# Kernel tuning notes

Hardware: AMD Instinct MI355X
Metric: run time of the kernel (lower is better)

## Reference

```python
import jax, jax.numpy as jnp
import numpy as np
from jax import lax

B, H, W = 4, 512, 512
C_DOWN, C_UP = 256, 64
DH = DW = 32          # bottleneck feature map (H/16)
K = 512               # fixed proposal count per image (<= proposal_n_max)
NMS_THR = 0.2
MIN_DIST = 3
PROP_HALF = 5         # proposal_size(11) // 2
POOL = 7
NCLS = 4              # n_classes(3) + background


def leaky(x):
    return jnp.where(x > 0, x, 0.1 * x)


def setup_inputs() -> dict:
    key = jax.random.key(0)
    ks = jax.random.split(key, 12)
    s = lambda fan: np.float32(1.0 / np.sqrt(fan))
    return {
        "xhat": jax.random.uniform(ks[0], (B, 1, H, W), jnp.float32),
        "feat_down": jax.random.normal(ks[1], (B, C_DOWN, DH, DW), jnp.float32),
        "feat_up": jax.random.normal(ks[2], (B, C_UP, H, W), jnp.float32),
        # patch head: per-pixel => only 3x3 conv center taps contribute
        "pw1": jax.random.normal(ks[3], (256, C_DOWN), jnp.float32) * s(C_DOWN),
        "pb1": jnp.zeros((256,), jnp.float32),
        "pw2": jax.random.normal(ks[4], (256, 256), jnp.float32) * s(256),
        "pb2": jnp.zeros((256,), jnp.float32),
        "pw3": jax.random.normal(ks[5], (256, 256), jnp.float32) * s(256),
        "pb3": jnp.zeros((256,), jnp.float32),
        "pfc_w": jax.random.normal(ks[6], (2, 256), jnp.float32) * s(256),
        "pfc_b": jnp.zeros((2,), jnp.float32),
        # proposal head: full 3x3 convs on 7x7 pooled rois
        "qw1": jax.random.normal(ks[7], (256, C_UP, 3, 3), jnp.float32) * s(C_UP * 9),
        "qb1": jnp.zeros((256,), jnp.float32),
        "qw2": jax.random.normal(ks[8], (256, 256, 3, 3), jnp.float32) * s(256 * 9),
        "qb2": jnp.zeros((256,), jnp.float32),
        "qw3": jax.random.normal(ks[9], (256, 256, 3, 3), jnp.float32) * s(256 * 9),
        "qb3": jnp.zeros((256,), jnp.float32),
        "qfc_w": jax.random.normal(ks[10], (NCLS, 256), jnp.float32) * s(256),
        "qfc_b": jnp.zeros((NCLS,), jnp.float32),
    }


def reference(xhat, feat_down, feat_up, pw1, pb1, pw2, pb2, pw3, pb3, pfc_w, pfc_b,
              qw1, qb1, qw2, qb2, qw3, qb3, qfc_w, qfc_b):
    # ---- patch classifier applied per pixel (3x3 conv on 1x1 padded input == center tap)
    f = leaky(jnp.einsum('bchw,oc->bohw', feat_down, pw1) + pb1[None, :, None, None])
    f = leaky(jnp.einsum('bchw,oc->bohw', f, pw2) + pb2[None, :, None, None])
    f = leaky(jnp.einsum('bchw,oc->bohw', f, pw3) + pb3[None, :, None, None])
    plogits = jnp.einsum('bchw,oc->bohw', f, pfc_w) + pfc_b[None, :, None, None]
    patch_score = jax.nn.softmax(plogits, axis=1)[:, 1:2]                 # [B,1,DH,DW]
    patch_score = jax.image.resize(patch_score, (B, 1, H, W), 'bilinear')  # align_corners=False
    # gate belief map: bad pixels set to global mean of bad pixels
    bad = patch_score < 0.5
    nbad = jnp.maximum(jnp.sum(bad), 1).astype(xhat.dtype)
    mean_bad = jnp.sum(jnp.where(bad, xhat, 0.0)) / nbad
    bm = jnp.where(bad, mean_bad, xhat)[:, 0]                             # [B,H,W]
    # ---- belief-map NMS: local maxima above absolute threshold
    win = 2 * MIN_DIST + 1
    mp = lax.reduce_window(bm, -jnp.inf, lax.max, (1, win, win), (1, 1, 1), 'SAME')
    peak_scores = jnp.where((bm == mp) & (bm > NMS_THR), bm, -jnp.inf)
    top_s, top_i = lax.top_k(peak_scores.reshape(B, -1), K)               # [B,K]
    ys = (top_i // W).astype(jnp.int32)
    xs = (top_i % W).astype(jnp.int32)
    valid = top_s > NMS_THR
    coords = jnp.stack([xs, ys], axis=-1)                                 # (x, y)
    # ---- roi_align: 11x11 boxes around peaks, one bilinear sample per 7x7 bin center
    roi_size = 2.0 * PROP_HALF
    offs = (jnp.arange(POOL, dtype=jnp.float32) + 0.5) * (roi_size / POOL)
    px = (xs.astype(jnp.float32) - PROP_HALF)[..., None] + offs           # [B,K,7]
    py = (ys.astype(jnp.float32) - PROP_HALF)[..., None] + offs

    def sample_one(feat, py_i, px_i):
        # feat [C,H,W]; py_i/px_i [K,7] -> pooled [C,K,7,7]
        yy = jnp.broadcast_to(py_i[:, :, None], (K, POOL, POOL))
        xx = jnp.broadcast_to(px_i[:, None, :], (K, POOL, POOL))
        y0 = jnp.floor(yy); x0 = jnp.floor(xx)
        wy = yy - y0; wx = xx - x0
        y0i = jnp.clip(y0.astype(jnp.int32), 0, H - 1)
        y1i = jnp.clip(y0.astype(jnp.int32) + 1, 0, H - 1)
        x0i = jnp.clip(x0.astype(jnp.int32), 0, W - 1)
        x1i = jnp.clip(x0.astype(jnp.int32) + 1, 0, W - 1)
        g = lambda yi, xi: feat[:, yi, xi]
        return (g(y0i, x0i) * (1 - wy) * (1 - wx) + g(y0i, x1i) * (1 - wy) * wx
                + g(y1i, x0i) * wy * (1 - wx) + g(y1i, x1i) * wy * wx)

    pooled = jax.vmap(sample_one)(feat_up, py, px)                        # [B,C,K,7,7]
    pooled = pooled.transpose(0, 2, 1, 3, 4).reshape(B * K, C_UP, POOL, POOL)
    # ---- proposal classifier head
    dn = ('NCHW', 'OIHW', 'NCHW')
    h = leaky(lax.conv_general_dilated(pooled, qw1, (1, 1), 'SAME', dimension_numbers=dn) + qb1[None, :, None, None])
    h = leaky(lax.conv_general_dilated(h, qw2, (1, 1), 'SAME', dimension_numbers=dn) + qb2[None, :, None, None])
    h = leaky(lax.conv_general_dilated(h, qw3, (1, 1), 'SAME', dimension_numbers=dn) + qb3[None, :, None, None])
    h = jnp.max(h, axis=(2, 3))                                           # AdaptiveMaxPool2d(1)
    cls_logits = (h @ qfc_w.T + qfc_b).reshape(B, K, NCLS)
    return cls_logits, coords, top_s, valid
```

## Files before the change

### kernel.cpp

```cpp
#include <hip/hip_runtime.h>
#include <math.h>

typedef _Float16 half_t;
typedef half_t half8 __attribute__((ext_vector_type(8)));
typedef half_t half4 __attribute__((ext_vector_type(4)));
typedef float  f32x16 __attribute__((ext_vector_type(16)));
typedef double dbl2  __attribute__((ext_vector_type(2)));

#define BB 4
#define HH 512
#define WW 512
#define IMGPIX (HH*WW)
#define KSEL 512
#define NPROP (BB*KSEL)
#define CUP 64
#define NMS_THR 0.2f

#define OFF_S32    0
#define OFF_SUM    32768
#define OFF_CNT    32776
#define OFF_CCNT   32784
#define OFF_HIST   32800
#define ZERO_BASE  32768
#define ZERO_LEN   262176
#define OFF_PFX    294944
#define OFF_R      294976
#define OFF_BITMAP 295040
#define OFF_KEYS   426112
#define OFF_SEL    8814720
#define OFF_PROPS  8831104
#define OFF_W1     8847488
#define OFF_W2     9142400
#define OFF_W3     10322048

#define LRELU_F(x) ((x) > 0.0f ? (x) : 0.1f*(x))

__global__ __launch_bounds__(256) void repatch_k(
    const float* __restrict__ fdown,
    const float* __restrict__ pw1, const float* __restrict__ pb1,
    const float* __restrict__ pw2, const float* __restrict__ pb2,
    const float* __restrict__ pw3, const float* __restrict__ pb3,
    const float* __restrict__ pfcw, const float* __restrict__ pfcb,
    double* __restrict__ s32,
    const float* __restrict__ qw1, const float* __restrict__ qw2,
    const float* __restrict__ qw3,
    half_t* __restrict__ W1, half_t* __restrict__ W2, half_t* __restrict__ W3)
{
  if (blockIdx.x >= 512) {
    const int tot1 = 256*64*9, tot2 = 256*256*9;
    int idx = (blockIdx.x - 512)*256 + threadIdx.x;
    const float* src; half_t* dst; int IC, KS, l;
    if (idx < tot1)              { src = qw1; dst = W1; IC = 64;  KS = 4;  l = idx; }
    else if (idx < tot1 + tot2)  { src = qw2; dst = W2; IC = 256; KS = 16; l = idx - tot1; }
    else if (idx < tot1 + 2*tot2){ src = qw3; dst = W3; IC = 256; KS = 16; l = idx - tot1 - tot2; }
    else return;
    int tap = l % 9;
    int t   = l / 9;
    int ic  = t % IC;
    int oc  = t / IC;
    int ks  = ic >> 4, kin = ic & 15;
    dst[((size_t)(tap*KS + ks)*256 + oc)*16 + kin] = (half_t)src[l];
    return;
  }
  __shared__ __align__(16) double xb[8][256];
  const int t = threadIdx.x;
  const int base_px = blockIdx.x * 8;
#pragma unroll
  for (int p = 0; p < 8; ++p) {
    int px = base_px + p;
    int b = px >> 10, rem = px & 1023;
    xb[p][t] = (double)fdown[(size_t)(b*256 + t)*1024 + rem];
  }
  __syncthreads();
  const float* Ws[3] = {pw1, pw2, pw3};
  const float* Bs[3] = {pb1, pb2, pb3};
  for (int L = 0; L < 3; ++L) {
    double acc[8];
    double bias = (double)Bs[L][t];
#pragma unroll
    for (int p = 0; p < 8; ++p) acc[p] = bias;
    const float* wrow = Ws[L] + t*256;
    for (int c = 0; c < 256; c += 2) {
      double w0 = (double)wrow[c], w1 = (double)wrow[c+1];
#pragma unroll
      for (int p = 0; p < 8; ++p) {
        dbl2 xv = *(const dbl2*)&xb[p][c];
        acc[p] += w0 * xv.x;
        acc[p] += w1 * xv.y;
      }
    }
    __syncthreads();
#pragma unroll
    for (int p = 0; p < 8; ++p)
      xb[p][t] = acc[p] > 0.0 ? acc[p] : 0.1*acc[p];
    __syncthreads();
  }
  if (t < 8) {
    double l0 = (double)pfcb[0], l1 = (double)pfcb[1];
    for (int c = 0; c < 256; ++c) {
      double xv = xb[t][c];
      l0 += (double)pfcw[c]       * xv;
      l1 += (double)pfcw[256 + c] * xv;
    }
    double m  = fmax(l0, l1);
    double e0 = exp(l0 - m), e1 = exp(l1 - m);
    s32[base_px + t] = e1 / (e0 + e1);
  }
}

__device__ __forceinline__ double upsample_ps(const double* __restrict__ s32,
                                              int b, int oy, int ox)
{
  double sy = (oy + 0.5)*0.0625 - 0.5;
  double sx = (ox + 0.5)*0.0625 - 0.5;
  double fy = floor(sy), fx = floor(sx);
  double wy = sy - fy,   wx = sx - fx;
  int y0 = (int)fy, x0 = (int)fx;
  int y0i = min(max(y0,   0), 31), y1i = min(max(y0+1, 0), 31);
  int x0i = min(max(x0,   0), 31), x1i = min(max(x0+1, 0), 31);
  const double* s = s32 + b*1024;
  double v00 = s[y0i*32+x0i], v01 = s[y0i*32+x1i];
  double v10 = s[y1i*32+x0i], v11 = s[y1i*32+x1i];
  return v00*(1.0-wy)*(1.0-wx) + v01*(1.0-wy)*wx
       + v10*wy*(1.0-wx)       + v11*wy*wx;
}

__global__ __launch_bounds__(256) void mean_k(
    const float* __restrict__ xhat, const double* __restrict__ s32,
    double* __restrict__ sum, unsigned long long* __restrict__ cnt,
    unsigned long long* __restrict__ bitmap)
{
  int id = blockIdx.x*256 + threadIdx.x;
  int b = id >> 18, rem = id & (IMGPIX-1);
  int oy = rem >> 9, ox = rem & 511;
  double ps = upsample_ps(s32, b, oy, ox);
  bool bad = ps < 0.5;
  int lane = threadIdx.x & 63;
  unsigned long long bb = __ballot(bad);
  if (lane == 0) bitmap[id >> 6] = bb;
  double v = bad ? (double)xhat[id] : 0.0;
  int    c = bad ? 1 : 0;
  for (int off = 32; off; off >>= 1) {
    v += __shfl_down(v, off);
    c += __shfl_down(c, off);
  }
  __shared__ double sv[4];
  __shared__ int    sc[4];
  int w = threadIdx.x >> 6;
  if (lane == 0) { sv[w] = v; sc[w] = c; }
  __syncthreads();
  if (threadIdx.x == 0) {
    atomicAdd(sum, sv[0]+sv[1]+sv[2]+sv[3]);
    atomicAdd(cnt, (unsigned long long)(sc[0]+sc[1]+sc[2]+sc[3]));
  }
}

__global__ __launch_bounds__(512) void keyfuse_k(
    const float* __restrict__ xhat, const unsigned long long* __restrict__ bitmap,
    const double* __restrict__ sum, const unsigned long long* __restrict__ cnt,
    unsigned long long* __restrict__ keys, unsigned int* __restrict__ hist0)
{
  __shared__ float rowm[14][512];
  __shared__ float bmv[8][512];
  __shared__ float rt[512];
  __shared__ unsigned int lh[4096];
  const int tid = threadIdx.x;
  const int img = blockIdx.x >> 6;
  const int rb  = (blockIdx.x & 63) * 8;
  for (int i = tid; i < 4096; i += 512) lh[i] = 0;

  unsigned long long n = *cnt; if (n < 1) n = 1;
  const float mean = (float)(*sum / (double)n);
  const int ibase = img * IMGPIX;

  for (int r = 0; r < 14; ++r) {
    int y = rb - 3 + r;
    float v = -INFINITY;
    if (y >= 0 && y < 512) {
      int id = ibase + (y << 9) + tid;
      bool bad = (bitmap[id >> 6] >> (id & 63)) & 1ull;
      v = bad ? mean : xhat[id];
    }
    int cr = y - rb;
    if (cr >= 0 && cr < 8) bmv[cr][tid] = v;
    rt[tid] = v;
    __syncthreads();
    int lo = max(tid-3, 0), hi = min(tid+3, 511);
    float m = rt[lo];
    for (int xx = lo+1; xx <= hi; ++xx) m = fmaxf(m, rt[xx]);
    rowm[r][tid] = m;
    __syncthreads();
  }

  const int lane = tid & 63;
  for (int yy = 0; yy < 8; ++yy) {
    float mp = rowm[yy][tid];
#pragma unroll
    for (int d = 1; d < 7; ++d) mp = fmaxf(mp, rowm[yy + d][tid]);
    float v = bmv[yy][tid];
    bool cand = (v == mp) && (v > NMS_THR);
    int rem = ((rb + yy) << 9) + tid;
    unsigned int inv = (unsigned int)((IMGPIX-1) - rem);
    unsigned long long key = cand
        ? ((((unsigned long long)__float_as_uint(v)) << 18) | inv)
        : (unsigned long long)inv;
    keys[ibase + rem] = key;
    int bin = (int)(key >> 36);
    unsigned long long active = ~0ull;
    while (active) {
      int src = __ffsll((long long)active) - 1;
      int bsel = __shfl(bin, src);
      unsigned long long match = __ballot(bin == bsel) & active;
      if (lane == src) atomicAdd(&lh[bsel], (unsigned int)__popcll(match));
      active &= ~match;
    }
  }
  __syncthreads();
  for (int i = tid; i < 4096; i += 512)
    if (lh[i]) atomicAdd(&hist0[img*4096 + i], lh[i]);
}

__global__ __launch_bounds__(512) void hist_k(
    const unsigned long long* __restrict__ keys,
    const unsigned long long* __restrict__ pfx,
    unsigned int* __restrict__ hist, int shift)
{
  __shared__ unsigned int lh[4096];
  const int tid = threadIdx.x;
  for (int i = tid; i < 4096; i += 512) lh[i] = 0;
  int id = blockIdx.x*512 + tid;
  int img = blockIdx.x >> 9;
  unsigned long long key = keys[id];
  bool pred = (key >> (shift + 12)) == pfx[img];
  int bin = (int)((unsigned int)(key >> shift) & 4095u);
  __syncthreads();
  int lane = tid & 63;
  unsigned long long active = __ballot(pred);
  while (active) {
    int src = __ffsll((long long)active) - 1;
    int bsel = __shfl(bin, src);
    unsigned long long match = __ballot(bin == bsel) & active;
    if (lane == src) atomicAdd(&lh[bsel], (unsigned int)__popcll(match));
    active &= ~match;
  }
  __syncthreads();
  for (int i = tid; i < 4096; i += 512)
    if (lh[i]) atomicAdd(&hist[img*4096 + i], lh[i]);
}

__global__ __launch_bounds__(512) void scan_k(
    const unsigned int* __restrict__ hist,
    unsigned long long* __restrict__ pfx, unsigned int* __restrict__ Rbuf,
    int pass)
{
  __shared__ unsigned int lsA[512], lsB[512];
  const int b = blockIdx.x, tid = threadIdx.x;
  unsigned long long pin = (pass == 0) ? 0ull : pfx[b];
  unsigned int Rin = (pass == 0) ? (unsigned int)KSEL : Rbuf[b];
  const unsigned int* h = hist + b*4096;
  unsigned int v[8]; unsigned int loc = 0;
#pragma unroll
  for (int j = 0; j < 8; ++j) { v[j] = h[tid*8 + j]; loc += v[j]; }
  lsA[tid] = loc;
  __syncthreads();
  unsigned int* s = lsA; unsigned int* d = lsB;
  for (int dd = 1; dd < 512; dd <<= 1) {
    unsigned int val = s[tid] + ((tid + dd < 512) ? s[tid + dd] : 0u);
    d[tid] = val;
    __syncthreads();
    unsigned int* t = s; s = d; d = t;
  }
  unsigned int nxt = (tid + 1 < 512) ? s[tid + 1] : 0u;
#pragma unroll
  for (int j = 7; j >= 0; --j) {
    unsigned int sfx = nxt + v[j];
    if (sfx >= Rin && nxt < Rin) {
      pfx[b] = (pin << 12) | (unsigned long long)(unsigned int)(tid*8 + j);
      Rbuf[b] = Rin - nxt;
    }
    nxt = sfx;
  }
}

__global__ __launch_bounds__(512) void collect_k(
    const unsigned long long* __restrict__ keys,
    const unsigned long long* __restrict__ pfx,
    unsigned int* __restrict__ ccnt, unsigned long long* __restrict__ sel)
{
  int id = blockIdx.x*512 + threadIdx.x;
  int img = blockIdx.x >> 9;
  unsigned long long key = keys[id];
  if (key >= pfx[img]) {
    unsigned int pos = atomicAdd(&ccnt[img], 1u);
    if (pos < 512) sel[img*512 + pos] = key;
  }
}

__global__ __launch_bounds__(512) void sortout_k(
    const unsigned long long* __restrict__ sel,
    float* __restrict__ out, int* __restrict__ props)
{
  __shared__ unsigned long long s[512];
  const int b = blockIdx.x, tid = threadIdx.x;
  s[tid] = sel[b*512 + tid];
  __syncthreads();
  for (int size = 2; size <= 512; size <<= 1) {
    for (int stride = size >> 1; stride > 0; stride >>= 1) {
      int j = tid ^ stride;
      if (j > tid) {
        unsigned long long a = s[tid], c = s[j];
        bool up = ((tid & size) == 0);
        if (up ? (a < c) : (a > c)) { s[tid] = c; s[j] = a; }
      }
      __syncthreads();
    }
  }
  unsigned long long k = s[tid];
  unsigned int fbits = (unsigned int)(k >> 18);
  int idx = (IMGPIX-1) - (int)(k & 0x3FFFFull);
  int y = idx >> 9, x = idx & 511;
  float val = fbits ? __uint_as_float(fbits) : -INFINITY;
  int slot = (b << 9) + tid;
  out[12288 + slot]       = val;
  out[8192 + slot*2 + 0]  = (float)x;
  out[8192 + slot*2 + 1]  = (float)y;
  out[14336 + slot]       = (val > NMS_THR) ? 1.0f : 0.0f;
  props[slot*2 + 0] = x;
  props[slot*2 + 1] = y;
}

#define SA2 264
#define SA1 72

template<int KS, int SA>
__device__ __forceinline__ void conv32(
    const half_t* __restrict__ Wl, const half_t* __restrict__ Xin,
    int prop, int mtb, int l31, int lh, f32x16 acc[2][2])
{
#pragma unroll
  for (int mt = 0; mt < 2; ++mt)
#pragma unroll
    for (int nt = 0; nt < 2; ++nt)
#pragma unroll
      for (int r = 0; r < 16; ++r) acc[mt][nt][r] = 0.f;

  for (int tap = 0; tap < 9; ++tap) {
    const int dy = tap/3 - 1, dx = tap%3 - 1;
    int xb[2];
#pragma unroll
    for (int nt = 0; nt < 2; ++nt) {
      int px = nt*32 + l31;
      int y = px/7, x = px - y*7;
      int yy = y + dy, xx = x + dx;
      bool valid = (px < 49) & (yy >= 0) & (yy < 7) & (xx >= 0) & (xx < 7);
      int row = valid ? (prop*49 + yy*7 + xx) : 98;
      xb[nt] = row*SA + lh*8;
    }
    const half_t* wb = Wl + ((size_t)(tap*KS)*256 + mtb + l31)*16 + lh*8;
#pragma unroll 4
    for (int ks = 0; ks < KS; ++ks) {
      half8 b0 = *(const half8*)(Xin + xb[0] + ks*16);
      half8 b1 = *(const half8*)(Xin + xb[1] + ks*16);
      half8 a0 = *(const half8*)(wb + (ks*256      )*16);
      half8 a1 = *(const half8*)(wb + (ks*256 + 32 )*16);
      acc[0][0] = __builtin_amdgcn_mfma_f32_32x32x16_f16(a0, b0, acc[0][0], 0,0,0);
      acc[0][1] = __builtin_amdgcn_mfma_f32_32x32x16_f16(a0, b1, acc[0][1], 0,0,0);
      acc[1][0] = __builtin_amdgcn_mfma_f32_32x32x16_f16(a1, b0, acc[1][0], 0,0,0);
      acc[1][1] = __builtin_amdgcn_mfma_f32_32x32x16_f16(a1, b1, acc[1][1], 0,0,0);
    }
  }
}

__device__ __forceinline__ void store32(
    half_t* __restrict__ X2, const float* __restrict__ bias,
    int prop, int mtb, int ntb, int l31, int lh, const f32x16& a)
{
  int px = ntb + l31;
  if (px >= 49) return;
  half_t* dst = X2 + (prop*49 + px)*SA2;
  int oc0 = mtb + 4*lh;
#pragma unroll
  for (int q = 0; q < 4; ++q) {
    int oc = oc0 + 8*q;
    half4 h;
#pragma unroll
    for (int r = 0; r < 4; ++r) {
      float v = a[4*q + r] + bias[oc + r];
      h[r] = (half_t)LRELU_F(v);
    }
    *(half4*)(dst + oc) = h;
  }
}

__global__ __launch_bounds__(512, 4) void head_k(
    const float* __restrict__ fup, const int* __restrict__ props,
    const half_t* __restrict__ W1, const half_t* __restrict__ W2,
    const half_t* __restrict__ W3,
    const float* __restrict__ qb1, const float* __restrict__ qb2,
    const float* __restrict__ qb3,
    const float* __restrict__ qfcw, const float* __restrict__ qfcb,
    float* __restrict__ out)
{
  __shared__ __align__(16) half_t X2[99*SA2];
  __shared__ __align__(16) char  U[99*SA1*2];
  half_t* X1 = (half_t*)U;
  float*  S  = (float*)U;

  const int p0 = blockIdx.x*2;
  const int b  = p0 >> 9;
  const int tid = threadIdx.x;
  const int w = tid >> 6, lane = tid & 63;
  const int l31 = lane & 31, lh = lane >> 5;
  const int mg = w & 3, ng = w >> 2;
  const int mtb = mg*64;

  for (int i = tid; i < SA2; i += 512) X2[98*SA2 + i] = (half_t)0.f;
  for (int i = tid; i < SA1; i += 512) X1[98*SA1 + i] = (half_t)0.f;

  const float step = (float)(10.0/7.0);
  for (int it = tid; it < 2*CUP*49; it += 512) {
    int pp = it / (CUP*49), rem2 = it - pp*(CUP*49);
    int c = rem2 / 49, bin = rem2 - c*49;
    int iy = bin / 7, ix = bin - iy*7;
    int cx = props[2*(p0+pp)], cy = props[2*(p0+pp)+1];
    float fy = ((float)cy - 5.0f) + ((float)iy + 0.5f)*step;
    float fx = ((float)cx - 5.0f) + ((float)ix + 0.5f)*step;
    float y0f = floorf(fy), x0f = floorf(fx);
    float wy = fy - y0f,    wx = fx - x0f;
    int y0 = (int)y0f, x0 = (int)x0f;
    int y0i = min(max(y0,   0), 511), y1i = min(max(y0+1, 0), 511);
    int x0i = min(max(x0,   0), 511), x1i = min(max(x0+1, 0), 511);
    const float* f = fup + ((size_t)(b*CUP + c) << 18);
    float v00 = f[(y0i<<9)+x0i], v01 = f[(y0i<<9)+x1i];
    float v10 = f[(y1i<<9)+x0i], v11 = f[(y1i<<9)+x1i];
    float v = v00*(1.f-wy)*(1.f-wx) + v01*(1.f-wy)*wx
            + v10*wy*(1.f-wx)       + v11*wy*wx;
    X1[(pp*49 + iy*7 + ix)*SA1 + c] = (half_t)v;
  }
  __syncthreads();

  f32x16 acc[2][2];

  conv32<4, SA1>(W1, X1, ng, mtb, l31, lh, acc);
#pragma unroll
  for (int mt = 0; mt < 2; ++mt)
#pragma unroll
    for (int nt = 0; nt < 2; ++nt)
      store32(X2, qb1, ng, mtb + mt*32, nt*32, l31, lh, acc[mt][nt]);
  __syncthreads();

  conv32<16, SA2>(W2, X2, ng, mtb, l31, lh, acc);
  __syncthreads();
#pragma unroll
  for (int mt = 0; mt < 2; ++mt)
#pragma unroll
    for (int nt = 0; nt < 2; ++nt)
      store32(X2, qb2, ng, mtb + mt*32, nt*32, l31, lh, acc[mt][nt]);
  __syncthreads();

  conv32<16, SA2>(W3, X2, ng, mtb, l31, lh, acc);
#pragma unroll
  for (int mt = 0; mt < 2; ++mt) {
#pragma unroll
    for (int q = 0; q < 4; ++q) {
#pragma unroll
      for (int r = 0; r < 4; ++r) {
        int oc = mtb + mt*32 + 8*q + 4*lh + r;
        float bv = qb3[oc];
        float m = LRELU_F(acc[mt][0][4*q + r] + bv);
        if (l31 < 17) {
          float v2 = LRELU_F(acc[mt][1][4*q + r] + bv);
          m = fmaxf(m, v2);
        }
#pragma unroll
        for (int d = 1; d < 32; d <<= 1) m = fmaxf(m, __shfl_xor(m, d));
        if (l31 == 0) S[ng*256 + oc] = m;
      }
    }
  }
  __syncthreads();

  float* P = (float*)X2;
  {
    int pj = tid >> 8, oc = tid & 255;
    float h = S[pj*256 + oc];
#pragma unroll
    for (int j = 0; j < 4; ++j) P[(pj*4 + j)*256 + oc] = h * qfcw[j*256 + oc];
  }
  __syncthreads();
  {
    int sseg = tid >> 6, o = tid & 63;
    float v = P[sseg*256 + o] + P[sseg*256 + o + 64]
            + P[sseg*256 + o + 128] + P[sseg*256 + o + 192];
#pragma unroll
    for (int d = 1; d < 64; d <<= 1) v += __shfl_xor(v, d);
    if (o == 0) {
      int pg = p0 + (sseg >> 2), j = sseg & 3;
      out[pg*4 + j] = v + qfcb[j];
    }
  }
}

extern "C" void kernel_launch(void* const* d_in, const int* in_sizes, int n_in,
                              void* d_out, int out_size, void* d_ws, size_t ws_size,
                              hipStream_t stream)
{
  (void)in_sizes; (void)n_in; (void)out_size; (void)ws_size;
  const float* xhat  = (const float*)d_in[0];
  const float* fdown = (const float*)d_in[1];
  const float* fup   = (const float*)d_in[2];
  const float* pw1   = (const float*)d_in[3];
  const float* pb1   = (const float*)d_in[4];
  const float* pw2   = (const float*)d_in[5];
  const float* pb2   = (const float*)d_in[6];
  const float* pw3   = (const float*)d_in[7];
  const float* pb3   = (const float*)d_in[8];
  const float* pfcw  = (const float*)d_in[9];
  const float* pfcb  = (const float*)d_in[10];
  const float* qw1   = (const float*)d_in[11];
  const float* qb1   = (const float*)d_in[12];
  const float* qw2   = (const float*)d_in[13];
  const float* qb2   = (const float*)d_in[14];
  const float* qw3   = (const float*)d_in[15];
  const float* qb3   = (const float*)d_in[16];
  const float* qfcw  = (const float*)d_in[17];
  const float* qfcb  = (const float*)d_in[18];

  char* ws = (char*)d_ws;
  double*             s32   = (double*)(ws + OFF_S32);
  double*             sum   = (double*)(ws + OFF_SUM);
  unsigned long long* cnt   = (unsigned long long*)(ws + OFF_CNT);
  unsigned int*       ccnt  = (unsigned int*)(ws + OFF_CCNT);
  unsigned int*       hist  = (unsigned int*)(ws + OFF_HIST);
  unsigned long long* pfx   = (unsigned long long*)(ws + OFF_PFX);
  unsigned int*       Rbuf  = (unsigned int*)(ws + OFF_R);
  unsigned long long* bmap  = (unsigned long long*)(ws + OFF_BITMAP);
  unsigned long long* keys  = (unsigned long long*)(ws + OFF_KEYS);
  unsigned long long* sel   = (unsigned long long*)(ws + OFF_SEL);
  int*                props = (int*)(ws + OFF_PROPS);
  half_t*             Wp1   = (half_t*)(ws + OFF_W1);
  half_t*             Wp2   = (half_t*)(ws + OFF_W2);
  half_t*             Wp3   = (half_t*)(ws + OFF_W3);
  float*              out   = (float*)d_out;

  hipMemsetAsync(ws + ZERO_BASE, 0, ZERO_LEN, stream);

  const int repack_blocks = (256*64*9 + 2*256*256*9 + 255)/256;
  repatch_k<<<512 + repack_blocks, 256, 0, stream>>>(
      fdown, pw1,pb1, pw2,pb2, pw3,pb3, pfcw,pfcb, s32,
      qw1, qw2, qw3, Wp1, Wp2, Wp3);

  mean_k   <<<4096, 256, 0, stream>>>(xhat, s32, sum, cnt, bmap);
  keyfuse_k<<<256, 512, 0, stream>>>(xhat, bmap, sum, cnt, keys, hist + 0*4*4096);
  scan_k   <<<BB, 512, 0, stream>>>(hist + 0*4*4096, pfx, Rbuf, 0);
  hist_k   <<<2048, 512, 0, stream>>>(keys, pfx, hist + 1*4*4096, 24);
  scan_k   <<<BB, 512, 0, stream>>>(hist + 1*4*4096, pfx, Rbuf, 1);
  hist_k   <<<2048, 512, 0, stream>>>(keys, pfx, hist + 2*4*4096, 12);
  scan_k   <<<BB, 512, 0, stream>>>(hist + 2*4*4096, pfx, Rbuf, 2);
  hist_k   <<<2048, 512, 0, stream>>>(keys, pfx, hist + 3*4*4096, 0);
  scan_k   <<<BB, 512, 0, stream>>>(hist + 3*4*4096, pfx, Rbuf, 3);
  collect_k<<<2048, 512, 0, stream>>>(keys, pfx, ccnt, sel);
  sortout_k<<<BB, 512, 0, stream>>>(sel, out, props);

  head_k   <<<NPROP/2, 512, 0, stream>>>(fup, props, Wp1, Wp2, Wp3,
                                         qb1, qb2, qb3, qfcw, qfcb, out);
}
```

Before: 950.3 us.

## Split ROI bilinear sampling into separate kernel and fully unroll conv taps

Moves the bilinear ROI pooling out of the MFMA head kernel into a dedicated roi_k kernel. It writes fp16 pooled features to a workspace buffer that reuses the now-dead bitmap/keys region, and head_k then copies them into LDS with vector loads. This is meant to stop latency-bound scattered gathers from stalling the matrix-core kernel. It also precomputes per-tap LDS offsets, fully unrolls the 9 taps with a deeper inner unroll, and relaxes launch bounds to 2 blocks per CU to allow more registers. The cost is an extra kernel launch, a global round trip of the pooled tensor, and possibly lower occupancy.

```diff
diff --git a/kernel.cpp b/kernel.cpp
--- a/kernel.cpp
+++ b/kernel.cpp
@@ -27,11 +27,12 @@
 #define OFF_R      294976
 #define OFF_BITMAP 295040
 #define OFF_KEYS   426112
-#define OFF_SEL    8814720
-#define OFF_PROPS  8831104
-#define OFF_W1     8847488
-#define OFF_W2     9142400
-#define OFF_W3     10322048
+#define OFF_X1G    295040
+#define OFF_SEL    13140096
+#define OFF_PROPS  13156480
+#define OFF_W1     13172864
+#define OFF_W2     13467776
+#define OFF_W3     14647424
 
 #define LRELU_F(x) ((x) > 0.0f ? (x) : 0.1f*(x))
 
@@ -329,100 +330,17 @@
   props[slot*2 + 1] = y;
 }
 
-#define SA2 264
-#define SA1 72
-
-template<int KS, int SA>
-__device__ __forceinline__ void conv32(
-    const half_t* __restrict__ Wl, const half_t* __restrict__ Xin,
-    int prop, int mtb, int l31, int lh, f32x16 acc[2][2])
-{
-#pragma unroll
-  for (int mt = 0; mt < 2; ++mt)
-#pragma unroll
-    for (int nt = 0; nt < 2; ++nt)
-#pragma unroll
-      for (int r = 0; r < 16; ++r) acc[mt][nt][r] = 0.f;
-
-  for (int tap = 0; tap < 9; ++tap) {
-    const int dy = tap/3 - 1, dx = tap%3 - 1;
-    int xb[2];
-#pragma unroll
-    for (int nt = 0; nt < 2; ++nt) {
-      int px = nt*32 + l31;
-      int y = px/7, x = px - y*7;
-      int yy = y + dy, xx = x + dx;
-      bool valid = (px < 49) & (yy >= 0) & (yy < 7) & (xx >= 0) & (xx < 7);
-      int row = valid ? (prop*49 + yy*7 + xx) : 98;
-      xb[nt] = row*SA + lh*8;
-    }
-    const half_t* wb = Wl + ((size_t)(tap*KS)*256 + mtb + l31)*16 + lh*8;
-#pragma unroll 4
-    for (int ks = 0; ks < KS; ++ks) {
-      half8 b0 = *(const half8*)(Xin + xb[0] + ks*16);
-      half8 b1 = *(const half8*)(Xin + xb[1] + ks*16);
-      half8 a0 = *(const half8*)(wb + (ks*256      )*16);
-      half8 a1 = *(const half8*)(wb + (ks*256 + 32 )*16);
-      acc[0][0] = __builtin_amdgcn_mfma_f32_32x32x16_f16(a0, b0, acc[0][0], 0,0,0);
-      acc[0][1] = __builtin_amdgcn_mfma_f32_32x32x16_f16(a0, b1, acc[0][1], 0,0,0);
-      acc[1][0] = __builtin_amdgcn_mfma_f32_32x32x16_f16(a1, b0, acc[1][0], 0,0,0);
-      acc[1][1] = __builtin_amdgcn_mfma_f32_32x32x16_f16(a1, b1, acc[1][1], 0,0,0);
-    }
-  }
-}
-
-__device__ __forceinline__ void store32(
-    half_t* __restrict__ X2, const float* __restrict__ bias,
-    int prop, int mtb, int ntb, int l31, int lh, const f32x16& a)
-{
-  int px = ntb + l31;
-  if (px >= 49) return;
-  half_t* dst = X2 + (prop*49 + px)*SA2;
-  int oc0 = mtb + 4*lh;
-#pragma unroll
-  for (int q = 0; q < 4; ++q) {
-    int oc = oc0 + 8*q;
-    half4 h;
-#pragma unroll
-    for (int r = 0; r < 4; ++r) {
-      float v = a[4*q + r] + bias[oc + r];
-      h[r] = (half_t)LRELU_F(v);
-    }
-    *(half4*)(dst + oc) = h;
-  }
-}
-
-__global__ __launch_bounds__(512, 4) void head_k(
+__global__ __launch_bounds__(256) void roi_k(
     const float* __restrict__ fup, const int* __restrict__ props,
-    const half_t* __restrict__ W1, const half_t* __restrict__ W2,
-    const half_t* __restrict__ W3,
-    const float* __restrict__ qb1, const float* __restrict__ qb2,
-    const float* __restrict__ qb3,
-    const float* __restrict__ qfcw, const float* __restrict__ qfcb,
-    float* __restrict__ out)
-{
-  __shared__ __align__(16) half_t X2[99*SA2];
-  __shared__ __align__(16) char  U[99*SA1*2];
-  half_t* X1 = (half_t*)U;
-  float*  S  = (float*)U;
-
-  const int p0 = blockIdx.x*2;
-  const int b  = p0 >> 9;
-  const int tid = threadIdx.x;
-  const int w = tid >> 6, lane = tid & 63;
-  const int l31 = lane & 31, lh = lane >> 5;
-  const int mg = w & 3, ng = w >> 2;
-  const int mtb = mg*64;
-
-  for (int i = tid; i < SA2; i += 512) X2[98*SA2 + i] = (half_t)0.f;
-  for (int i = tid; i < SA1; i += 512) X1[98*SA1 + i] = (half_t)0.f;
-
+    half_t* __restrict__ X1g)
+{
+  const int p  = blockIdx.x;
+  const int b  = p >> 9;
+  const int cx = props[2*p], cy = props[2*p+1];
   const float step = (float)(10.0/7.0);
-  for (int it = tid; it < 2*CUP*49; it += 512) {
-    int pp = it / (CUP*49), rem2 = it - pp*(CUP*49);
-    int c = rem2 / 49, bin = rem2 - c*49;
+  for (int it = threadIdx.x; it < CUP*49; it += 256) {
+    int c = it / 49, bin = it - c*49;
     int iy = bin / 7, ix = bin - iy*7;
-    int cx = props[2*(p0+pp)], cy = props[2*(p0+pp)+1];
     float fy = ((float)cy - 5.0f) + ((float)iy + 0.5f)*step;
     float fx = ((float)cx - 5.0f) + ((float)ix + 0.5f)*step;
     float y0f = floorf(fy), x0f = floorf(fx);
@@ -435,7 +353,112 @@
     float v10 = f[(y1i<<9)+x0i], v11 = f[(y1i<<9)+x1i];
     float v = v00*(1.f-wy)*(1.f-wx) + v01*(1.f-wy)*wx
             + v10*wy*(1.f-wx)       + v11*wy*wx;
-    X1[(pp*49 + iy*7 + ix)*SA1 + c] = (half_t)v;
+    X1g[(size_t)p*3136 + bin*64 + c] = (half_t)v;
+  }
+}
+
+#define SA2 264
+#define SA1 72
+
+template<int KS, int SA>
+__device__ __forceinline__ void conv32(
+    const half_t* __restrict__ Wl, const half_t* __restrict__ Xin,
+    int prop, int mtb, int l31, int lh, f32x16 acc[2][2])
+{
+#pragma unroll
+  for (int mt = 0; mt < 2; ++mt)
+#pragma unroll
+    for (int nt = 0; nt < 2; ++nt)
+#pragma unroll
+      for (int r = 0; r < 16; ++r) acc[mt][nt][r] = 0.f;
+
+  int xb0[9], xb1[9];
+#pragma unroll
+  for (int tap = 0; tap < 9; ++tap) {
+    const int dy = tap/3 - 1, dx = tap%3 - 1;
+#pragma unroll
+    for (int nt = 0; nt < 2; ++nt) {
+      int px = nt*32 + l31;
+      int y = px/7, x = px - y*7;
+      int yy = y + dy, xx = x + dx;
+      bool valid = (px < 49) & (yy >= 0) & (yy < 7) & (xx >= 0) & (xx < 7);
+      int row = valid ? (prop*49 + yy*7 + xx) : 98;
+      int v = row*SA + lh*8;
+      if (nt == 0) xb0[tap] = v; else xb1[tap] = v;
+    }
+  }
+
+  const half_t* wb = Wl + ((size_t)mtb + l31)*16 + lh*8;
+#pragma unroll
+  for (int tap = 0; tap < 9; ++tap) {
+    const half_t* wt = wb + (size_t)tap*KS*256*16;
+#pragma unroll 8
+    for (int ks = 0; ks < KS; ++ks) {
+      half8 b0 = *(const half8*)(Xin + xb0[tap] + ks*16);
+      half8 b1 = *(const half8*)(Xin + xb1[tap] + ks*16);
+      half8 a0 = *(const half8*)(wt + (ks*256      )*16);
+      half8 a1 = *(const half8*)(wt + (ks*256 + 32 )*16);
+      acc[0][0] = __builtin_amdgcn_mfma_f32_32x32x16_f16(a0, b0, acc[0][0], 0,0,0);
+      acc[0][1] = __builtin_amdgcn_mfma_f32_32x32x16_f16(a0, b1, acc[0][1], 0,0,0);
+      acc[1][0] = __builtin_amdgcn_mfma_f32_32x32x16_f16(a1, b0, acc[1][0], 0,0,0);
+      acc[1][1] = __builtin_amdgcn_mfma_f32_32x32x16_f16(a1, b1, acc[1][1], 0,0,0);
+    }
+  }
+}
+
+__device__ __forceinline__ void store32(
+    half_t* __restrict__ X2, const float* __restrict__ bias,
+    int prop, int mtb, int ntb, int l31, int lh, const f32x16& a)
+{
+  int px = ntb + l31;
+  if (px >= 49) return;
+  half_t* dst = X2 + (prop*49 + px)*SA2;
+  int oc0 = mtb + 4*lh;
+#pragma unroll
+  for (int q = 0; q < 4; ++q) {
+    int oc = oc0 + 8*q;
+    half4 h;
+#pragma unroll
+    for (int r = 0; r < 4; ++r) {
+      float v = a[4*q + r] + bias[oc + r];
+      h[r] = (half_t)LRELU_F(v);
+    }
+    *(half4*)(dst + oc) = h;
+  }
+}
+
+__global__ __launch_bounds__(512, 2) void head_k(
+    const half_t* __restrict__ X1g, const int* __restrict__ props,
+    const half_t* __restrict__ W1, const half_t* __restrict__ W2,
+    const half_t* __restrict__ W3,
+    const float* __restrict__ qb1, const float* __restrict__ qb2,
+    const float* __restrict__ qb3,
+    const float* __restrict__ qfcw, const float* __restrict__ qfcb,
+    float* __restrict__ out)
+{
+  __shared__ __align__(16) half_t X2[99*SA2];
+  __shared__ __align__(16) char  U[99*SA1*2];
+  half_t* X1 = (half_t*)U;
+  float*  S  = (float*)U;
+
+  const int p0 = blockIdx.x*2;
+  const int tid = threadIdx.x;
+  const int w = tid >> 6, lane = tid & 63;
+  const int l31 = lane & 31, lh = lane >> 5;
+  const int mg = w & 3, ng = w >> 2;
+  const int mtb = mg*64;
+  (void)props;
+
+  for (int i = tid; i < SA2; i += 512) X2[98*SA2 + i] = (half_t)0.f;
+  for (int i = tid; i < SA1; i += 512) X1[98*SA1 + i] = (half_t)0.f;
+
+  for (int i = tid; i < 784; i += 512) {
+    int pp  = i / 392;
+    int r2  = i - pp*392;
+    int row = r2 >> 3;
+    int cc  = (r2 & 7) * 8;
+    half8 v = *(const half8*)(X1g + (size_t)(p0+pp)*3136 + row*64 + cc);
+    *(half8*)(X1 + (pp*49 + row)*SA1 + cc) = v;
   }
   __syncthreads();
 
@@ -536,6 +559,7 @@
   unsigned int*       Rbuf  = (unsigned int*)(ws + OFF_R);
   unsigned long long* bmap  = (unsigned long long*)(ws + OFF_BITMAP);
   unsigned long long* keys  = (unsigned long long*)(ws + OFF_KEYS);
+  half_t*             X1g   = (half_t*)(ws + OFF_X1G);
   unsigned long long* sel   = (unsigned long long*)(ws + OFF_SEL);
   int*                props = (int*)(ws + OFF_PROPS);
   half_t*             Wp1   = (half_t*)(ws + OFF_W1);
@@ -562,6 +586,7 @@
   collect_k<<<2048, 512, 0, stream>>>(keys, pfx, ccnt, sel);
   sortout_k<<<BB, 512, 0, stream>>>(sel, out, props);
 
-  head_k   <<<NPROP/2, 512, 0, stream>>>(fup, props, Wp1, Wp2, Wp3,
+  roi_k    <<<NPROP, 256, 0, stream>>>(fup, props, X1g);
+  head_k   <<<NPROP/2, 512, 0, stream>>>(X1g, props, Wp1, Wp2, Wp3,
                                          qb1, qb2, qb3, qfcw, qfcb, out);
 }
```

Result: slower. 1.049 ms (+10.3%).

## Widen per-wave MFMA tile to 128 output channels and halve head block size

Applied to the files above, without the earlier changes.

The proposal head kernel now runs 4 waves per block instead of 8. Each wave computes a 128x64 output tile (4x2 MFMA accumulators) instead of 64x64, so every B-operand load from shared memory feeds twice as many MFMAs. Tap offsets are precomputed and the tap loop is fully unrolled. The intent is to reduce LDS traffic per MFMA and raise the compute-to-load ratio. In exchange, accumulator registers double to 128 per lane, which may lower occupancy or cause spills, and fewer waves are left to hide weight-load latency.

```diff
diff --git a/kernel.cpp b/kernel.cpp
--- a/kernel.cpp
+++ b/kernel.cpp
@@ -335,18 +335,19 @@
 template<int KS, int SA>
 __device__ __forceinline__ void conv32(
     const half_t* __restrict__ Wl, const half_t* __restrict__ Xin,
-    int prop, int mtb, int l31, int lh, f32x16 acc[2][2])
-{
-#pragma unroll
-  for (int mt = 0; mt < 2; ++mt)
+    int prop, int mtb, int l31, int lh, f32x16 acc[4][2])
+{
+#pragma unroll
+  for (int mt = 0; mt < 4; ++mt)
 #pragma unroll
     for (int nt = 0; nt < 2; ++nt)
 #pragma unroll
       for (int r = 0; r < 16; ++r) acc[mt][nt][r] = 0.f;
 
+  int xb0[9], xb1[9];
+#pragma unroll
   for (int tap = 0; tap < 9; ++tap) {
     const int dy = tap/3 - 1, dx = tap%3 - 1;
-    int xb[2];
 #pragma unroll
     for (int nt = 0; nt < 2; ++nt) {
       int px = nt*32 + l31;
@@ -354,19 +355,32 @@
       int yy = y + dy, xx = x + dx;
       bool valid = (px < 49) & (yy >= 0) & (yy < 7) & (xx >= 0) & (xx < 7);
       int row = valid ? (prop*49 + yy*7 + xx) : 98;
-      xb[nt] = row*SA + lh*8;
-    }
-    const half_t* wb = Wl + ((size_t)(tap*KS)*256 + mtb + l31)*16 + lh*8;
-#pragma unroll 4
+      int v = row*SA + lh*8;
+      if (nt == 0) xb0[tap] = v; else xb1[tap] = v;
+    }
+  }
+
+  const half_t* wb = Wl + ((size_t)mtb + l31)*16 + lh*8;
+#pragma unroll
+  for (int tap = 0; tap < 9; ++tap) {
+    const half_t* wt = wb + (size_t)tap*KS*256*16;
+#pragma unroll 2
     for (int ks = 0; ks < KS; ++ks) {
-      half8 b0 = *(const half8*)(Xin + xb[0] + ks*16);
-      half8 b1 = *(const half8*)(Xin + xb[1] + ks*16);
-      half8 a0 = *(const half8*)(wb + (ks*256      )*16);
-      half8 a1 = *(const half8*)(wb + (ks*256 + 32 )*16);
+      half8 b0 = *(const half8*)(Xin + xb0[tap] + ks*16);
+      half8 b1 = *(const half8*)(Xin + xb1[tap] + ks*16);
+      const half_t* wk = wt + (size_t)ks*256*16;
+      half8 a0 = *(const half8*)(wk);
+      half8 a1 = *(const half8*)(wk + 32*16);
+      half8 a2 = *(const half8*)(wk + 64*16);
+      half8 a3 = *(const half8*)(wk + 96*16);
       acc[0][0] = __builtin_amdgcn_mfma_f32_32x32x16_f16(a0, b0, acc[0][0], 0,0,0);
       acc[0][1] = __builtin_amdgcn_mfma_f32_32x32x16_f16(a0, b1, acc[0][1], 0,0,0);
       acc[1][0] = __builtin_amdgcn_mfma_f32_32x32x16_f16(a1, b0, acc[1][0], 0,0,0);
       acc[1][1] = __builtin_amdgcn_mfma_f32_32x32x16_f16(a1, b1, acc[1][1], 0,0,0);
+      acc[2][0] = __builtin_amdgcn_mfma_f32_32x32x16_f16(a2, b0, acc[2][0], 0,0,0);
+      acc[2][1] = __builtin_amdgcn_mfma_f32_32x32x16_f16(a2, b1, acc[2][1], 0,0,0);
+      acc[3][0] = __builtin_amdgcn_mfma_f32_32x32x16_f16(a3, b0, acc[3][0], 0,0,0);
+      acc[3][1] = __builtin_amdgcn_mfma_f32_32x32x16_f16(a3, b1, acc[3][1], 0,0,0);
     }
   }
 }
@@ -392,7 +406,7 @@
   }
 }
 
-__global__ __launch_bounds__(512, 4) void head_k(
+__global__ __launch_bounds__(256, 2) void head_k(
     const float* __restrict__ fup, const int* __restrict__ props,
     const half_t* __restrict__ W1, const half_t* __restrict__ W2,
     const half_t* __restrict__ W3,
@@ -411,14 +425,14 @@
   const int tid = threadIdx.x;
   const int w = tid >> 6, lane = tid & 63;
   const int l31 = lane & 31, lh = lane >> 5;
-  const int mg = w & 3, ng = w >> 2;
-  const int mtb = mg*64;
-
-  for (int i = tid; i < SA2; i += 512) X2[98*SA2 + i] = (half_t)0.f;
-  for (int i = tid; i < SA1; i += 512) X1[98*SA1 + i] = (half_t)0.f;
+  const int mg = w & 1, ng = w >> 1;
+  const int mtb = mg*128;
+
+  for (int i = tid; i < SA2; i += 256) X2[98*SA2 + i] = (half_t)0.f;
+  for (int i = tid; i < SA1; i += 256) X1[98*SA1 + i] = (half_t)0.f;
 
   const float step = (float)(10.0/7.0);
-  for (int it = tid; it < 2*CUP*49; it += 512) {
+  for (int it = tid; it < 2*CUP*49; it += 256) {
     int pp = it / (CUP*49), rem2 = it - pp*(CUP*49);
     int c = rem2 / 49, bin = rem2 - c*49;
     int iy = bin / 7, ix = bin - iy*7;
@@ -439,11 +453,11 @@
   }
   __syncthreads();
 
-  f32x16 acc[2][2];
+  f32x16 acc[4][2];
 
   conv32<4, SA1>(W1, X1, ng, mtb, l31, lh, acc);
 #pragma unroll
-  for (int mt = 0; mt < 2; ++mt)
+  for (int mt = 0; mt < 4; ++mt)
 #pragma unroll
     for (int nt = 0; nt < 2; ++nt)
       store32(X2, qb1, ng, mtb + mt*32, nt*32, l31, lh, acc[mt][nt]);
@@ -452,7 +466,7 @@
   conv32<16, SA2>(W2, X2, ng, mtb, l31, lh, acc);
   __syncthreads();
 #pragma unroll
-  for (int mt = 0; mt < 2; ++mt)
+  for (int mt = 0; mt < 4; ++mt)
 #pragma unroll
     for (int nt = 0; nt < 2; ++nt)
       store32(X2, qb2, ng, mtb + mt*32, nt*32, l31, lh, acc[mt][nt]);
@@ -460,7 +474,7 @@
 
   conv32<16, SA2>(W3, X2, ng, mtb, l31, lh, acc);
 #pragma unroll
-  for (int mt = 0; mt < 2; ++mt) {
+  for (int mt = 0; mt < 4; ++mt) {
 #pragma unroll
     for (int q = 0; q < 4; ++q) {
 #pragma unroll
@@ -481,21 +495,21 @@
   __syncthreads();
 
   float* P = (float*)X2;
-  {
-    int pj = tid >> 8, oc = tid & 255;
-    float h = S[pj*256 + oc];
-#pragma unroll
-    for (int j = 0; j < 4; ++j) P[(pj*4 + j)*256 + oc] = h * qfcw[j*256 + oc];
-  }
-  __syncthreads();
-  {
-    int sseg = tid >> 6, o = tid & 63;
-    float v = P[sseg*256 + o] + P[sseg*256 + o + 64]
-            + P[sseg*256 + o + 128] + P[sseg*256 + o + 192];
+#pragma unroll
+  for (int pp = 0; pp < 2; ++pp) {
+    float h = S[pp*256 + tid];
+#pragma unroll
+    for (int j = 0; j < 4; ++j) P[(pp*4 + j)*256 + tid] = h * qfcw[j*256 + tid];
+  }
+  __syncthreads();
+  for (int sg = tid >> 6; sg < 8; sg += 4) {
+    int o = tid & 63;
+    float v = P[sg*256 + o] + P[sg*256 + o + 64]
+            + P[sg*256 + o + 128] + P[sg*256 + o + 192];
 #pragma unroll
     for (int d = 1; d < 64; d <<= 1) v += __shfl_xor(v, d);
     if (o == 0) {
-      int pg = p0 + (sseg >> 2), j = sseg & 3;
+      int pg = p0 + (sg >> 2), j = sg & 3;
       out[pg*4 + j] = v + qfcb[j];
     }
   }
@@ -562,6 +576,6 @@
   collect_k<<<2048, 512, 0, stream>>>(keys, pfx, ccnt, sel);
   sortout_k<<<BB, 512, 0, stream>>>(sel, out, props);
 
-  head_k   <<<NPROP/2, 512, 0, stream>>>(fup, props, Wp1, Wp2, Wp3,
+  head_k   <<<NPROP/2, 256, 0, stream>>>(fup, props, Wp1, Wp2, Wp3,
                                          qb1, qb2, qb3, qfcw, qfcb, out);
 }
```

Result: slower. 1.059 ms (+11.4%).
